# Kernel optimization log

Hardware: AMD Instinct MI355X
Metric: run time of the kernel (lower is better)

## Reference

```python
import jax, jax.numpy as jnp
import numpy as np

BN_EPS = 1e-5


def _bn_relu(x, gamma, beta):
    # training-mode BatchNorm1d over (batch, length) per channel; x: [B,C,N]
    mean = jnp.mean(x, axis=(0, 2), keepdims=True)
    var = jnp.var(x, axis=(0, 2), keepdims=True)  # biased, matching torch normalization
    xh = (x - mean) * jax.lax.rsqrt(var + BN_EPS)
    return jax.nn.relu(xh * gamma[None, :, None] + beta[None, :, None])


def setup_inputs() -> dict:
    key = jax.random.key(0)
    ks = jax.random.split(key, 12)
    B, N, S, C1, C2 = 16, 4096, 1024, 256, 256
    C_in = C1 + C2  # 512
    M0, M1 = 256, 256  # mlp channels
    return {
        "xyz1": jax.random.normal(ks[0], (B, 3, N), dtype=jnp.float32),
        "xyz2": jax.random.normal(ks[1], (B, 3, S), dtype=jnp.float32),
        "points1": jax.random.normal(ks[2], (B, C1, N), dtype=jnp.float32),
        "points2": jax.random.normal(ks[3], (B, C2, S), dtype=jnp.float32),
        "w0": jax.random.normal(ks[4], (M0, C_in), dtype=jnp.float32) * 0.02,
        "b0": jnp.zeros((M0,), dtype=jnp.float32),
        "g0": jnp.ones((M0,), dtype=jnp.float32),
        "be0": jnp.zeros((M0,), dtype=jnp.float32),
        "w1": jax.random.normal(ks[5], (M1, M0), dtype=jnp.float32) * 0.02,
        "b1": jnp.zeros((M1,), dtype=jnp.float32),
        "g1": jnp.ones((M1,), dtype=jnp.float32),
        "be1": jnp.zeros((M1,), dtype=jnp.float32),
    }


def reference(xyz1, xyz2, points1, points2, w0, b0, g0, be0, w1, b1, g1, be1):
    # xyz1: [B,3,N], xyz2: [B,3,S], points1: [B,C1,N], points2: [B,C2,S]
    xyz1_t = xyz1.transpose(0, 2, 1)  # [B,N,3]
    xyz2_t = xyz2.transpose(0, 2, 1)  # [B,S,3]
    p2_t = points2.transpose(0, 2, 1)  # [B,S,C2]

    # squared pairwise distances [B,N,S] via |a|^2 + |b|^2 - 2ab
    d = (jnp.sum(xyz1_t ** 2, -1)[:, :, None]
         + jnp.sum(xyz2_t ** 2, -1)[:, None, :]
         - 2.0 * jnp.einsum('bnd,bsd->bns', xyz1_t, xyz2_t))

    # 3 nearest neighbours (smallest distances)
    neg_d3, idx = jax.lax.top_k(-d, 3)  # [B,N,3]
    dists = -neg_d3

    recip = 1.0 / (dists + 1e-8)
    weight = recip / jnp.sum(recip, axis=-1, keepdims=True)  # [B,N,3]

    gathered = jax.vmap(lambda p, i: p[i])(p2_t, idx)  # [B,N,3,C2]
    interp = jnp.sum(gathered * weight[..., None], axis=2)  # [B,N,C2]

    new_points = jnp.concatenate([points1.transpose(0, 2, 1), interp], axis=-1)  # [B,N,C1+C2]
    x = new_points.transpose(0, 2, 1)  # [B,C_in,N]

    # 1x1 Conv1d == per-position matmul
    x = _bn_relu(jnp.einsum('oi,bin->bon', w0, x) + b0[None, :, None], g0, be0)
    x = _bn_relu(jnp.einsum('oi,bin->bon', w1, x) + b1[None, :, None], g1, be1)
    return x
```

## Files before the change

kernel.cpp:

```cpp
#include <hip/hip_runtime.h>
#include <stdint.h>

using u16 = unsigned short;
using short8 = __attribute__((ext_vector_type(8))) short;
using ushort8 = __attribute__((ext_vector_type(8))) unsigned short;
using f32x4  = __attribute__((ext_vector_type(4))) float;
using u32x4  = __attribute__((ext_vector_type(4))) unsigned int;

__device__ __forceinline__ float bf2f(u16 u) {
  return __builtin_bit_cast(float, ((unsigned)u) << 16);
}
__device__ __forceinline__ u16 f2bf(float f) {
  unsigned u = __builtin_bit_cast(unsigned, f);
  u += 0x7FFFu + ((u >> 16) & 1u);
  return (u16)(u >> 16);
}
__device__ __forceinline__ unsigned bn2(unsigned w, float a0, float s0, float a1, float s1) {
  float f0 = bf2f((u16)(w & 0xFFFFu)) * a0 + s0;
  float f1 = bf2f((u16)(w >> 16))     * a1 + s1;
  f0 = f0 > 0.0f ? f0 : 0.0f;
  f1 = f1 > 0.0f ? f1 : 0.0f;
  return (unsigned)f2bf(f0) | ((unsigned)f2bf(f1) << 16);
}
__device__ __forceinline__ void bnprep_to_lds(
    const float* __restrict__ in_sums, const float* __restrict__ in_sumsq,
    const float* __restrict__ g, const float* __restrict__ be,
    float* sc_s, float* sh_s, int t) {
  if (t < 256) {
    float s = 0.0f, q = 0.0f;
    for (int k = 0; k < 8; ++k) { s += in_sums[k*256 + t]; q += in_sumsq[k*256 + t]; }
    const float inv_n = 1.0f / 65536.0f;
    float mean = s * inv_n;
    float var = q * inv_n - mean*mean;
    float a = g[t] * rsqrtf(var + 1e-5f);
    sc_s[t] = a;
    sh_s[t] = be[t] - mean * a;
  }
}

__device__ __forceinline__ void ins3(float& d0, float& d1, float& d2,
                                     int& i0, int& i1, int& i2, float d, int s) {
  bool c0 = d < d0, c1 = d < d1, c2 = d < d2;
  d2 = c1 ? d1 : (c2 ? d : d2);
  i2 = c1 ? i1 : (c2 ? s : i2);
  d1 = c0 ? d0 : (c1 ? d : d1);
  i1 = c0 ? i0 : (c1 ? s : i1);
  d0 = c0 ? d : d0;
  i0 = c0 ? s : i0;
}

__global__ __launch_bounds__(256, 8) void nn3_kernel(
    const float* __restrict__ xyz1, const float* __restrict__ xyz2,
    int* __restrict__ idx_out, float* __restrict__ w_out) {
  __shared__ __align__(16) float cand[8 * 516];
  const int b = blockIdx.y;
  const int t = threadIdx.x;
  const float* x2 = xyz2 + b * 3072;
  for (int i = t; i < 1024; i += 256) {
    float x = x2[i], y = x2[1024 + i], z = x2[2048 + i];
    f32x4 v = { -2.0f * x, -2.0f * y, -2.0f * z, x*x + y*y + z*z };
    *(f32x4*)&cand[(i >> 7) * 516 + (i & 127) * 4] = v;
  }
  __syncthreads();
  const int q = t >> 3, sub = t & 7;
  const int nA = blockIdx.x * 64 + q;
  const int nB = nA + 32;
  const float* x1 = xyz1 + b * 12288;
  const float pxA = x1[nA], pyA = x1[4096 + nA], pzA = x1[8192 + nA];
  const float pxB = x1[nB], pyB = x1[4096 + nB], pzB = x1[8192 + nB];
  float dA0 = 1e30f, dA1 = 1e30f, dA2 = 1e30f;
  float dB0 = 1e30f, dB1 = 1e30f, dB2 = 1e30f;
  int iA0 = 0, iA1 = 0, iA2 = 0, iB0 = 0, iB1 = 0, iB2 = 0;
  const int sbeg = sub << 7;
  const float* reg = &cand[sub * 516];
  #pragma unroll 2
  for (int ii = 0; ii < 128; ++ii) {
    f32x4 c = *(const f32x4*)(reg + ii * 4);
    float dA = __builtin_fmaf(pxA, c[0],
               __builtin_fmaf(pyA, c[1],
               __builtin_fmaf(pzA, c[2], c[3])));
    float dB = __builtin_fmaf(pxB, c[0],
               __builtin_fmaf(pyB, c[1],
               __builtin_fmaf(pzB, c[2], c[3])));
    ins3(dA0, dA1, dA2, iA0, iA1, iA2, dA, sbeg + ii);
    ins3(dB0, dB1, dB2, iB0, iB1, iB2, dB, sbeg + ii);
  }
  for (int st = 1; st <= 4; st <<= 1) {
    float e0 = __shfl_xor(dA0, st), e1 = __shfl_xor(dA1, st), e2 = __shfl_xor(dA2, st);
    int   j0 = __shfl_xor(iA0, st), j1 = __shfl_xor(iA1, st), j2 = __shfl_xor(iA2, st);
    ins3(dA0, dA1, dA2, iA0, iA1, iA2, e0, j0);
    ins3(dA0, dA1, dA2, iA0, iA1, iA2, e1, j1);
    ins3(dA0, dA1, dA2, iA0, iA1, iA2, e2, j2);
    float g0 = __shfl_xor(dB0, st), g1 = __shfl_xor(dB1, st), g2 = __shfl_xor(dB2, st);
    int   k0 = __shfl_xor(iB0, st), k1 = __shfl_xor(iB1, st), k2 = __shfl_xor(iB2, st);
    ins3(dB0, dB1, dB2, iB0, iB1, iB2, g0, k0);
    ins3(dB0, dB1, dB2, iB0, iB1, iB2, g1, k1);
    ins3(dB0, dB1, dB2, iB0, iB1, iB2, g2, k2);
  }
  if (sub == 0) {
    {
      const float r1 = pxA*pxA + pyA*pyA + pzA*pzA;
      float w0 = 1.0f/(dA0 + r1 + 1e-8f), w1 = 1.0f/(dA1 + r1 + 1e-8f), w2 = 1.0f/(dA2 + r1 + 1e-8f);
      float inv = 1.0f/(w0 + w1 + w2);
      const int pos = b * 4096 + nA;
      idx_out[pos*3+0] = iA0; idx_out[pos*3+1] = iA1; idx_out[pos*3+2] = iA2;
      w_out[pos*3+0] = w0*inv; w_out[pos*3+1] = w1*inv; w_out[pos*3+2] = w2*inv;
    }
    {
      const float r1 = pxB*pxB + pyB*pyB + pzB*pzB;
      float w0 = 1.0f/(dB0 + r1 + 1e-8f), w1 = 1.0f/(dB1 + r1 + 1e-8f), w2 = 1.0f/(dB2 + r1 + 1e-8f);
      float inv = 1.0f/(w0 + w1 + w2);
      const int pos = b * 4096 + nB;
      idx_out[pos*3+0] = iB0; idx_out[pos*3+1] = iB1; idx_out[pos*3+2] = iB2;
      w_out[pos*3+0] = w0*inv; w_out[pos*3+1] = w1*inv; w_out[pos*3+2] = w2*inv;
    }
  }
}

__global__ __launch_bounds__(256) void transpose2_cl(
    const float* __restrict__ in1, u16* __restrict__ out1,
    const float* __restrict__ in2, u16* __restrict__ out2) {
  __shared__ u16 tile[64][68];
  const int bx = blockIdx.x, b = blockIdx.z;
  const float* in; u16* out; int L, rstride, n0;
  if (bx < 64) { in = in1; out = out1; L = 4096; rstride = 512; n0 = bx * 64; }
  else         { in = in2; out = out2; L = 1024; rstride = 256; n0 = (bx - 64) * 64; }
  in  += (size_t)b * 256 * L;
  out += (size_t)b * L * rstride;
  const int c0 = blockIdx.y * 64;
  const int t = threadIdx.x;
  const int ci = t >> 4;
  const int nb = (t & 15) * 4;
  #pragma unroll
  for (int p = 0; p < 4; ++p) {
    const int cc = p*16 + ci;
    f32x4 v = *(const f32x4*)&in[(size_t)(c0 + cc) * L + n0 + nb];
    tile[nb+0][cc] = f2bf(v[0]);
    tile[nb+1][cc] = f2bf(v[1]);
    tile[nb+2][cc] = f2bf(v[2]);
    tile[nb+3][cc] = f2bf(v[3]);
  }
  __syncthreads();
  #pragma unroll
  for (int p = 0; p < 4; ++p) {
    const int nn = p*16 + ci;
    ushort4 o = *(const ushort4*)&tile[nn][nb];
    *(ushort4*)&out[(size_t)(n0 + nn) * rstride + c0 + nb] = o;
  }
}

__global__ __launch_bounds__(256) void cvt2_kernel(
    const float* __restrict__ a, u16* __restrict__ oa, int na,
    const float* __restrict__ b2, u16* __restrict__ ob, int nb) {
  int i = blockIdx.x * 256 + threadIdx.x;
  if (i < na) { oa[i] = f2bf(a[i]); }
  else { int j = i - na; if (j < nb) ob[j] = f2bf(b2[j]); }
}

__global__ __launch_bounds__(256) void interp_kernel(
    const u16* __restrict__ p2t, const int* __restrict__ idx,
    const float* __restrict__ wgt, u16* __restrict__ A1) {
  const int t = threadIdx.x;
  const int ln = t & 31, grp = t >> 5;
  const int c0 = ln * 8;
  for (int i = 0; i < 8; ++i) {
    const int pos = blockIdx.x * 64 + i * 8 + grp;
    const int b = pos >> 12;
    const int j0 = idx[pos*3+0], j1 = idx[pos*3+1], j2 = idx[pos*3+2];
    const float w0 = wgt[pos*3+0], w1 = wgt[pos*3+1], w2 = wgt[pos*3+2];
    ushort8 v0 = *(const ushort8*)(p2t + ((size_t)(b*1024 + j0)) * 256 + c0);
    ushort8 v1 = *(const ushort8*)(p2t + ((size_t)(b*1024 + j1)) * 256 + c0);
    ushort8 v2 = *(const ushort8*)(p2t + ((size_t)(b*1024 + j2)) * 256 + c0);
    ushort8 o;
    #pragma unroll
    for (int j = 0; j < 8; ++j)
      o[j] = f2bf(w0*bf2f(v0[j]) + w1*bf2f(v1[j]) + w2*bf2f(v2[j]));
    *(ushort8*)(A1 + (size_t)pos*512 + 256 + c0) = o;
  }
}

template <int FUSE>
__global__ __launch_bounds__(256) void gemm_kernel(
    const u16* __restrict__ A, const u16* __restrict__ Bw,
    const float* __restrict__ bias, u16* __restrict__ Y, int K,
    float* __restrict__ sums, float* __restrict__ sumsq,
    const float* __restrict__ in_sums, const float* __restrict__ in_sumsq,
    const float* __restrict__ g, const float* __restrict__ be) {
  __shared__ __align__(16) u16 As[128*72];
  __shared__ __align__(16) u16 Bs[128*72];
  __shared__ float sc_s[256], sh_s[256];
  const int t = threadIdx.x;
  const int m0 = blockIdx.x * 128, n0 = blockIdx.y * 128;
  const int wave = t >> 6, l = t & 63;
  const int wm = wave & 1, wn = wave >> 1;
  const int lc = l & 15, quad = l >> 4;
  f32x4 acc[4][4] = {};
  const int r = t >> 3, kc = (t & 7) * 8;
  if (FUSE) {
    bnprep_to_lds(in_sums, in_sumsq, g, be, sc_s, sh_s, t);
    __syncthreads();
  }
  for (int k0 = 0; k0 < K; k0 += 64) {
    f32x4 sc_lo, sc_hi, sh_lo, sh_hi;
    if (FUSE) {
      sc_lo = *(const f32x4*)&sc_s[k0 + kc];
      sc_hi = *(const f32x4*)&sc_s[k0 + kc + 4];
      sh_lo = *(const f32x4*)&sh_s[k0 + kc];
      sh_hi = *(const f32x4*)&sh_s[k0 + kc + 4];
    }
    #pragma unroll
    for (int p = 0; p < 4; ++p) {
      const int row = p*32 + r;
      u32x4 va = *(const u32x4*)&A [(size_t)(m0 + row)*K + k0 + kc];
      u32x4 vb = *(const u32x4*)&Bw[(size_t)(n0 + row)*K + k0 + kc];
      if (FUSE) {
        va[0] = bn2(va[0], sc_lo[0], sh_lo[0], sc_lo[1], sh_lo[1]);
        va[1] = bn2(va[1], sc_lo[2], sh_lo[2], sc_lo[3], sh_lo[3]);
        va[2] = bn2(va[2], sc_hi[0], sh_hi[0], sc_hi[1], sh_hi[1]);
        va[3] = bn2(va[3], sc_hi[2], sh_hi[2], sc_hi[3], sh_hi[3]);
      }
      *(u32x4*)&As[row*72 + kc] = va;
      *(u32x4*)&Bs[row*72 + kc] = vb;
    }
    __syncthreads();
    #pragma unroll
    for (int h = 0; h < 2; ++h) {
      short8 af[4], bfv[4];
      for (int tm = 0; tm < 4; ++tm)
        af[tm] = *(const short8*)&As[(wm*64 + tm*16 + lc)*72 + h*32 + quad*8];
      for (int tn = 0; tn < 4; ++tn)
        bfv[tn] = *(const short8*)&Bs[(wn*64 + tn*16 + lc)*72 + h*32 + quad*8];
      for (int tm = 0; tm < 4; ++tm)
        for (int tn = 0; tn < 4; ++tn)
          acc[tm][tn] = __builtin_amdgcn_mfma_f32_16x16x32_bf16(af[tm], bfv[tn], acc[tm][tn], 0, 0, 0);
    }
    __syncthreads();
  }
  float* sl = (float*)As;
  if (t < 256) sl[t] = 0.0f;
  __syncthreads();
  for (int tn = 0; tn < 4; ++tn) {
    const int colL = wn*64 + tn*16 + lc;
    const float bb = bias[n0 + colL];
    float s = 0.0f, q = 0.0f;
    for (int tm = 0; tm < 4; ++tm) {
      const int row = m0 + wm*64 + tm*16 + quad*4;
      for (int rr = 0; rr < 4; ++rr) {
        float v = acc[tm][tn][rr] + bb;
        Y[(size_t)(row + rr)*256 + n0 + colL] = f2bf(v);
        s += v; q += v*v;
      }
    }
    s += __shfl_xor(s, 16); s += __shfl_xor(s, 32);
    q += __shfl_xor(q, 16); q += __shfl_xor(q, 32);
    if (quad == 0) {
      atomicAdd(&sl[colL], s);
      atomicAdd(&sl[128 + colL], q);
    }
  }
  __syncthreads();
  if (t < 128) {
    const int bank = (blockIdx.x & 7) * 256;
    atomicAdd(&sums [bank + n0 + t], sl[t]);
    atomicAdd(&sumsq[bank + n0 + t], sl[128 + t]);
  }
}

__global__ __launch_bounds__(256) void bnrelu_tr_kernel(
    const u16* __restrict__ Y,
    const float* __restrict__ in_sums, const float* __restrict__ in_sumsq,
    const float* __restrict__ g, const float* __restrict__ be,
    float* __restrict__ out) {
  __shared__ u16 tile[64][266];
  __shared__ float sc_s[256], sh_s[256];
  const int t = threadIdx.x;
  const int b = blockIdx.z;
  const int n0 = blockIdx.x * 64;
  bnprep_to_lds(in_sums, in_sumsq, g, be, sc_s, sh_s, t);
  __syncthreads();
  const int ln = t & 63, grp = t >> 6;
  const int c0 = ln * 4;
  const f32x4 a4 = *(const f32x4*)&sc_s[c0];
  const f32x4 s4 = *(const f32x4*)&sh_s[c0];
  for (int it = 0; it < 16; ++it) {
    const int nn = it*4 + grp;
    size_t pos = (size_t)b*4096 + n0 + nn;
    ushort4 v = *(const ushort4*)&Y[pos*256 + c0];
    ushort4 o;
    float f0 = bf2f(v.x)*a4[0] + s4[0];
    float f1 = bf2f(v.y)*a4[1] + s4[1];
    float f2v = bf2f(v.z)*a4[2] + s4[2];
    float f3 = bf2f(v.w)*a4[3] + s4[3];
    o.x = f2bf(f0 > 0.0f ? f0 : 0.0f);
    o.y = f2bf(f1 > 0.0f ? f1 : 0.0f);
    o.z = f2bf(f2v > 0.0f ? f2v : 0.0f);
    o.w = f2bf(f3 > 0.0f ? f3 : 0.0f);
    *(ushort4*)&tile[nn][c0] = o;
  }
  __syncthreads();
  for (int p = 0; p < 32; ++p) {
    const int oo = p*8 + grp*2;
    ushort2 v = *(const ushort2*)&tile[ln][oo];
    out[((size_t)b*256 + oo    )*4096 + n0 + ln] = bf2f(v.x);
    out[((size_t)b*256 + oo + 1)*4096 + n0 + ln] = bf2f(v.y);
  }
}

extern "C" void kernel_launch(void* const* d_in, const int* in_sizes, int n_in,
                              void* d_out, int out_size, void* d_ws, size_t ws_size,
                              hipStream_t stream) {
  const float* xyz1    = (const float*)d_in[0];
  const float* xyz2    = (const float*)d_in[1];
  const float* points1 = (const float*)d_in[2];
  const float* points2 = (const float*)d_in[3];
  const float* w0      = (const float*)d_in[4];
  const float* b0      = (const float*)d_in[5];
  const float* g0      = (const float*)d_in[6];
  const float* be0     = (const float*)d_in[7];
  const float* w1      = (const float*)d_in[8];
  const float* b1      = (const float*)d_in[9];
  const float* g1      = (const float*)d_in[10];
  const float* be1     = (const float*)d_in[11];
  float* out = (float*)d_out;

  char* ws = (char*)d_ws;
  u16*   A1   = (u16*)ws;
  u16*   Y2   = (u16*)ws;
  u16*   Y    = (u16*)(ws + (64ull  << 20));
  u16*   p2t  = (u16*)(ws + (96ull  << 20));
  int*   idxb = (int*)(ws + (104ull << 20));
  float* wgtb = (float*)(ws + (105ull << 20));
  u16*   w0b  = (u16*)(ws + (106ull << 20));
  u16*   w1b  = (u16*)(ws + (106ull << 20) + (256u << 10));
  float* stats= (float*)(ws + (106ull << 20) + (512u << 10));

  float* sums0  = stats;
  float* sumsq0 = stats + 2048;
  float* sums1  = stats + 4096;
  float* sumsq1 = stats + 6144;

  hipMemsetAsync(stats, 0, 8192 * sizeof(float), stream);
  nn3_kernel<<<dim3(64, 16), 256, 0, stream>>>(xyz1, xyz2, idxb, wgtb);
  transpose2_cl<<<dim3(80, 4, 16), 256, 0, stream>>>(points1, A1, points2, p2t);
  cvt2_kernel<<<768, 256, 0, stream>>>(w0, w0b, 131072, w1, w1b, 65536);
  interp_kernel<<<1024, 256, 0, stream>>>(p2t, idxb, wgtb, A1);
  gemm_kernel<0><<<dim3(512, 2), 256, 0, stream>>>(A1, w0b, b0, Y, 512, sums0, sumsq0,
                                                   nullptr, nullptr, nullptr, nullptr);
  gemm_kernel<1><<<dim3(512, 2), 256, 0, stream>>>(Y, w1b, b1, Y2, 256, sums1, sumsq1,
                                                   sums0, sumsq0, g0, be0);
  bnrelu_tr_kernel<<<dim3(64, 1, 16), 256, 0, stream>>>(Y2, sums1, sumsq1, g1, be1, out);
}
```

Before: 288.8 us.

## Load GEMM MFMA fragments directly from global memory, dropping LDS staging

```diff
diff --git a/kernel.cpp b/kernel.cpp
--- a/kernel.cpp
+++ b/kernel.cpp
@@ -180,63 +180,58 @@
 }
 
 template <int FUSE>
-__global__ __launch_bounds__(256) void gemm_kernel(
+__global__ __launch_bounds__(256, 4) void gemm_kernel(
     const u16* __restrict__ A, const u16* __restrict__ Bw,
     const float* __restrict__ bias, u16* __restrict__ Y, int K,
     float* __restrict__ sums, float* __restrict__ sumsq,
     const float* __restrict__ in_sums, const float* __restrict__ in_sumsq,
     const float* __restrict__ g, const float* __restrict__ be) {
-  __shared__ __align__(16) u16 As[128*72];
-  __shared__ __align__(16) u16 Bs[128*72];
+  __shared__ float sl[256];
   __shared__ float sc_s[256], sh_s[256];
   const int t = threadIdx.x;
   const int m0 = blockIdx.x * 128, n0 = blockIdx.y * 128;
   const int wave = t >> 6, l = t & 63;
   const int wm = wave & 1, wn = wave >> 1;
   const int lc = l & 15, quad = l >> 4;
-  f32x4 acc[4][4] = {};
-  const int r = t >> 3, kc = (t & 7) * 8;
   if (FUSE) {
     bnprep_to_lds(in_sums, in_sumsq, g, be, sc_s, sh_s, t);
     __syncthreads();
   }
-  for (int k0 = 0; k0 < K; k0 += 64) {
-    f32x4 sc_lo, sc_hi, sh_lo, sh_hi;
+  f32x4 acc[4][4] = {};
+  const u16* aP[4]; const u16* bP[4];
+  #pragma unroll
+  for (int tm = 0; tm < 4; ++tm)
+    aP[tm] = &A [(size_t)(m0 + wm*64 + tm*16 + lc)*K + quad*8];
+  #pragma unroll
+  for (int tn = 0; tn < 4; ++tn)
+    bP[tn] = &Bw[(size_t)(n0 + wn*64 + tn*16 + lc)*K + quad*8];
+  #pragma unroll 4
+  for (int k0 = 0; k0 < K; k0 += 32) {
+    short8 af[4], bfv[4];
+    #pragma unroll
+    for (int tm = 0; tm < 4; ++tm) af[tm] = *(const short8*)(aP[tm] + k0);
+    #pragma unroll
+    for (int tn = 0; tn < 4; ++tn) bfv[tn] = *(const short8*)(bP[tn] + k0);
     if (FUSE) {
-      sc_lo = *(const f32x4*)&sc_s[k0 + kc];
-      sc_hi = *(const f32x4*)&sc_s[k0 + kc + 4];
-      sh_lo = *(const f32x4*)&sh_s[k0 + kc];
-      sh_hi = *(const f32x4*)&sh_s[k0 + kc + 4];
+      const int kb = k0 + quad*8;
+      f32x4 scA = *(const f32x4*)&sc_s[kb],   shA = *(const f32x4*)&sh_s[kb];
+      f32x4 scB = *(const f32x4*)&sc_s[kb+4], shB = *(const f32x4*)&sh_s[kb+4];
+      #pragma unroll
+      for (int tm = 0; tm < 4; ++tm) {
+        u32x4 w = __builtin_bit_cast(u32x4, af[tm]);
+        w[0] = bn2(w[0], scA[0], shA[0], scA[1], shA[1]);
+        w[1] = bn2(w[1], scA[2], shA[2], scA[3], shA[3]);
+        w[2] = bn2(w[2], scB[0], shB[0], scB[1], shB[1]);
+        w[3] = bn2(w[3], scB[2], shB[2], scB[3], shB[3]);
+        af[tm] = __builtin_bit_cast(short8, w);
+      }
     }
     #pragma unroll
-    for (int p = 0; p < 4; ++p) {
-      const int row = p*32 + r;
-      u32x4 va = *(const u32x4*)&A [(size_t)(m0 + row)*K + k0 + kc];
-      u32x4 vb = *(const u32x4*)&Bw[(size_t)(n0 + row)*K + k0 + kc];
-      if (FUSE) {
-        va[0] = bn2(va[0], sc_lo[0], sh_lo[0], sc_lo[1], sh_lo[1]);
-        va[1] = bn2(va[1], sc_lo[2], sh_lo[2], sc_lo[3], sh_lo[3]);
-        va[2] = bn2(va[2], sc_hi[0], sh_hi[0], sc_hi[1], sh_hi[1]);
-        va[3] = bn2(va[3], sc_hi[2], sh_hi[2], sc_hi[3], sh_hi[3]);
-      }
-      *(u32x4*)&As[row*72 + kc] = va;
-      *(u32x4*)&Bs[row*72 + kc] = vb;
-    }
-    __syncthreads();
-    #pragma unroll
-    for (int h = 0; h < 2; ++h) {
-      short8 af[4], bfv[4];
-      for (int tm = 0; tm < 4; ++tm)
-        af[tm] = *(const short8*)&As[(wm*64 + tm*16 + lc)*72 + h*32 + quad*8];
+    for (int tm = 0; tm < 4; ++tm)
+      #pragma unroll
       for (int tn = 0; tn < 4; ++tn)
-        bfv[tn] = *(const short8*)&Bs[(wn*64 + tn*16 + lc)*72 + h*32 + quad*8];
-      for (int tm = 0; tm < 4; ++tm)
-        for (int tn = 0; tn < 4; ++tn)
-          acc[tm][tn] = __builtin_amdgcn_mfma_f32_16x16x32_bf16(af[tm], bfv[tn], acc[tm][tn], 0, 0, 0);
-    }
-    __syncthreads();
-  }
-  float* sl = (float*)As;
+        acc[tm][tn] = __builtin_amdgcn_mfma_f32_16x16x32_bf16(af[tm], bfv[tn], acc[tm][tn], 0, 0, 0);
+  }
   if (t < 256) sl[t] = 0.0f;
   __syncthreads();
   for (int tn = 0; tn < 4; ++tn) {
```

After: 354.6 us. 22.8% more time.
